# Kernel optimization log

Measured on AMD Instinct MI355X. Metric: run time of the kernel, lower is better.

## Reference

```python
import jax, jax.numpy as jnp
import numpy as np

N_NODES = 100000
N_EDGES = 1600000
FEATURE = 128
HIDDEN = 128
CLASSES = 64


def _sage_conv(x, src, dst, W_l, b_l, W_r, num_nodes):
    # mean aggregation of source-node features at destination nodes
    msgs = x[src]                                            # [E, F]
    agg = jax.ops.segment_sum(msgs, dst, num_segments=num_nodes)   # [N, F]
    cnt = jax.ops.segment_sum(jnp.ones((src.shape[0],), x.dtype), dst,
                              num_segments=num_nodes)        # [N]
    mean = agg / jnp.maximum(cnt, 1.0)[:, None]              # zero for isolated nodes
    return mean @ W_l.T + b_l + x @ W_r.T


def setup_inputs() -> dict:
    key = jax.random.key(0)
    ks = jax.random.split(key, 8)
    x = jax.random.normal(ks[0], (N_NODES, FEATURE), dtype=jnp.float32)
    edge_index = jax.random.randint(ks[1], (2, N_EDGES), 0, N_NODES, dtype=jnp.int64)
    s1 = 1.0 / np.sqrt(FEATURE)
    s2 = 1.0 / np.sqrt(HIDDEN)
    W1l = jax.random.uniform(ks[2], (HIDDEN, FEATURE), jnp.float32, -s1, s1)
    b1l = jnp.zeros((HIDDEN,), jnp.float32)
    W1r = jax.random.uniform(ks[3], (HIDDEN, FEATURE), jnp.float32, -s1, s1)
    W2l = jax.random.uniform(ks[4], (CLASSES, HIDDEN), jnp.float32, -s2, s2)
    b2l = jnp.zeros((CLASSES,), jnp.float32)
    W2r = jax.random.uniform(ks[5], (CLASSES, HIDDEN), jnp.float32, -s2, s2)
    return {"x": x, "edge_index": edge_index,
            "W1l": W1l, "b1l": b1l, "W1r": W1r,
            "W2l": W2l, "b2l": b2l, "W2r": W2r}


def reference(x, edge_index, W1l, b1l, W1r, W2l, b2l, W2r):
    src, dst = edge_index[0], edge_index[1]
    h = _sage_conv(x, src, dst, W1l, b1l, W1r, N_NODES)
    h = jax.nn.relu(h)
    # F.dropout(training=False) is identity in eval mode
    out = _sage_conv(h, src, dst, W2l, b2l, W2r, N_NODES)
    return jax.nn.log_softmax(out, axis=1)
```

## Files before the change

### kernel.cpp

```cpp
#include <hip/hip_runtime.h>

#define NF 128
#define NC 64
#define NBA 640
#define NBKT 196
#define CAP 10240
#define CAPE 12288

typedef short short8 __attribute__((ext_vector_type(8)));
typedef unsigned short ushort;
typedef float f32x4 __attribute__((ext_vector_type(4)));
typedef float f32x2 __attribute__((ext_vector_type(2)));
typedef unsigned int uint;
typedef unsigned char uchar;

__device__ __forceinline__ ushort f2b(float x) {
  unsigned u = __builtin_bit_cast(unsigned, x);
  u += 0x7fffu + ((u >> 16) & 1u);
  return (ushort)(u >> 16);
}

__global__ __launch_bounds__(256) void prep_kernel(
    const float* __restrict__ x, ushort* __restrict__ xb,
    uchar* __restrict__ x8, int n4, int nb_cast,
    const float* __restrict__ W1l, const float* __restrict__ W1r,
    ushort* __restrict__ Wp1,
    const float* __restrict__ W2l, const float* __restrict__ W2r,
    ushort* __restrict__ Wp2l, ushort* __restrict__ Wp2r,
    const int* __restrict__ src, const int* __restrict__ dst,
    int* __restrict__ gcnt, uint* __restrict__ tmp, int nE, int epb) {
  __shared__ int lh[NBKT];
  __shared__ int base[NBKT];
  int b = blockIdx.x;
  if (b < nb_cast) {
    int i = b * 256 + threadIdx.x;
    if (i >= n4) return;
    float4 v = ((const float4*)x)[i];
    ushort4 o;
    o.x = f2b(v.x); o.y = f2b(v.y); o.z = f2b(v.z); o.w = f2b(v.w);
    ((ushort4*)xb)[i] = o;
    int u = __builtin_amdgcn_cvt_pk_fp8_f32(v.x, v.y, 0, false);
    u = __builtin_amdgcn_cvt_pk_fp8_f32(v.z, v.w, u, true);
    ((uint*)x8)[i] = (uint)u;
  } else if (b < nb_cast + 128) {
    int tid = (b - nb_cast) * 256 + threadIdx.x;
    int j = tid & 7;
    int lane = (tid >> 3) & 63;
    int tile = tid >> 9;
    int nt = tile & 7, kt = tile >> 3;
    int k = kt * 32 + ((lane >> 4) << 3) + j;
    int n = nt * 16 + (lane & 15);
    float v = (k < 128) ? W1l[n * 128 + k] : W1r[n * 128 + (k - 128)];
    Wp1[tid] = f2b(v);
  } else if (b < nb_cast + 192) {
    int tid0 = (b - nb_cast - 128) * 256 + threadIdx.x;
    int which = tid0 >> 13;
    int tid = tid0 & 8191;
    int j = tid & 7;
    int lane = (tid >> 3) & 63;
    int tile = tid >> 9;
    int nt = tile & 3, kt = tile >> 2;
    int k = kt * 32 + ((lane >> 4) << 3) + j;
    int n = nt * 16 + (lane & 15);
    const float* W = which ? W2r : W2l;
    ushort* Wp = which ? Wp2r : Wp2l;
    Wp[tid] = f2b(W[n * 128 + k]);
  } else {
    int blk = b - nb_cast - 192;
    const int t = threadIdx.x;
    for (int i = t; i < NBKT; i += 256) lh[i] = 0;
    __syncthreads();
    int s0 = blk * epb, s1 = min(nE, s0 + epb);
    for (int e = s0 + t; e < s1; e += 256) atomicAdd(&lh[dst[e] >> 9], 1);
    __syncthreads();
    for (int i = t; i < NBKT; i += 256) {
      int c = lh[i];
      base[i] = c ? atomicAdd(&gcnt[i], c) : 0;
      lh[i] = 0;
    }
    __syncthreads();
    for (int e = s0 + t; e < s1; e += 256) {
      int d = dst[e];
      int s = src[e];
      int bb = d >> 9;
      int r = atomicAdd(&lh[bb], 1);
      tmp[(size_t)bb * CAP + base[bb] + r] = ((uint)(d & 511) << 17) | (uint)s;
    }
  }
}

__global__ __launch_bounds__(256) void bsortB2_kernel(
    const uint* __restrict__ tmp, const int* __restrict__ gcnt,
    int* __restrict__ esrc, int* __restrict__ deg, int* __restrict__ off,
    int nN) {
  const int bkt = blockIdx.x;
  const int t = threadIdx.x;
  __shared__ int lh[512];
  __shared__ int cur[512];
  __shared__ int wsum[4];
  const int cnt = gcnt[bkt];
  const uint* tp = tmp + (size_t)bkt * CAP;
  const int ebase = bkt * CAPE;
  lh[t] = 0;
  lh[t + 256] = 0;
  __syncthreads();
  for (int i = t; i < cnt; i += 256) atomicAdd(&lh[tp[i] >> 17], 1);
  __syncthreads();
  int v0 = lh[2 * t], v1 = lh[2 * t + 1];
  int p0 = (v0 + 3) & ~3, p1 = (v1 + 3) & ~3;
  int ts = p0 + p1;
  int lane = t & 63, wid = t >> 6;
  int x = ts;
#pragma unroll
  for (int d = 1; d < 64; d <<= 1) {
    int y = __shfl_up(x, d);
    if (lane >= d) x += y;
  }
  if (lane == 63) wsum[wid] = x;
  __syncthreads();
  int wb = 0;
  for (int w = 0; w < wid; ++w) wb += wsum[w];
  int ex = wb + x - ts;
  cur[2 * t] = ex;
  cur[2 * t + 1] = ex + p0;
  int n0 = (bkt << 9) + 2 * t, n1 = n0 + 1;
  if (n0 < nN) { off[n0] = ebase + ex;      deg[n0] = v0; }
  if (n1 < nN) { off[n1] = ebase + ex + p0; deg[n1] = v1; }
  __syncthreads();
  for (int i = t; i < cnt; i += 256) {
    uint e = tp[i];
    int r = atomicAdd(&cur[e >> 17], 1);
    esrc[ebase + r] = (int)(e & 0x1FFFFu);
  }
}

__global__ __launch_bounds__(256) void gather1_kernel(
    const uchar* __restrict__ x8, const int* __restrict__ esrc,
    const int* __restrict__ off, const int* __restrict__ deg,
    ushort* __restrict__ aggm, int nN) {
  const int w = (blockIdx.x * blockDim.x + threadIdx.x) >> 4;
  const int l = threadIdx.x & 15;
  if (w >= nN) return;
  const int o = off[w];
  const int d = deg[w];
  const uint2* __restrict__ xp = (const uint2*)x8;
  f32x2 a0 = {}, a1 = {}, a2 = {}, a3 = {};
  int i = 0;
  for (; i + 8 <= d; i += 8) {
    int4 e0 = *(const int4*)(esrc + o + i);
    int4 e1 = *(const int4*)(esrc + o + i + 4);
    uint2 v0 = xp[(size_t)e0.x * 16 + l];
    uint2 v1 = xp[(size_t)e0.y * 16 + l];
    uint2 v2 = xp[(size_t)e0.z * 16 + l];
    uint2 v3 = xp[(size_t)e0.w * 16 + l];
    uint2 v4 = xp[(size_t)e1.x * 16 + l];
    uint2 v5 = xp[(size_t)e1.y * 16 + l];
    uint2 v6 = xp[(size_t)e1.z * 16 + l];
    uint2 v7 = xp[(size_t)e1.w * 16 + l];
    a0 += ((__builtin_amdgcn_cvt_pk_f32_fp8(v0.x, false) +
            __builtin_amdgcn_cvt_pk_f32_fp8(v1.x, false)) +
           (__builtin_amdgcn_cvt_pk_f32_fp8(v2.x, false) +
            __builtin_amdgcn_cvt_pk_f32_fp8(v3.x, false))) +
          ((__builtin_amdgcn_cvt_pk_f32_fp8(v4.x, false) +
            __builtin_amdgcn_cvt_pk_f32_fp8(v5.x, false)) +
           (__builtin_amdgcn_cvt_pk_f32_fp8(v6.x, false) +
            __builtin_amdgcn_cvt_pk_f32_fp8(v7.x, false)));
    a1 += ((__builtin_amdgcn_cvt_pk_f32_fp8(v0.x, true) +
            __builtin_amdgcn_cvt_pk_f32_fp8(v1.x, true)) +
           (__builtin_amdgcn_cvt_pk_f32_fp8(v2.x, true) +
            __builtin_amdgcn_cvt_pk_f32_fp8(v3.x, true))) +
          ((__builtin_amdgcn_cvt_pk_f32_fp8(v4.x, true) +
            __builtin_amdgcn_cvt_pk_f32_fp8(v5.x, true)) +
           (__builtin_amdgcn_cvt_pk_f32_fp8(v6.x, true) +
            __builtin_amdgcn_cvt_pk_f32_fp8(v7.x, true)));
    a2 += ((__builtin_amdgcn_cvt_pk_f32_fp8(v0.y, false) +
            __builtin_amdgcn_cvt_pk_f32_fp8(v1.y, false)) +
           (__builtin_amdgcn_cvt_pk_f32_fp8(v2.y, false) +
            __builtin_amdgcn_cvt_pk_f32_fp8(v3.y, false))) +
          ((__builtin_amdgcn_cvt_pk_f32_fp8(v4.y, false) +
            __builtin_amdgcn_cvt_pk_f32_fp8(v5.y, false)) +
           (__builtin_amdgcn_cvt_pk_f32_fp8(v6.y, false) +
            __builtin_amdgcn_cvt_pk_f32_fp8(v7.y, false)));
    a3 += ((__builtin_amdgcn_cvt_pk_f32_fp8(v0.y, true) +
            __builtin_amdgcn_cvt_pk_f32_fp8(v1.y, true)) +
           (__builtin_amdgcn_cvt_pk_f32_fp8(v2.y, true) +
            __builtin_amdgcn_cvt_pk_f32_fp8(v3.y, true))) +
          ((__builtin_amdgcn_cvt_pk_f32_fp8(v4.y, true) +
            __builtin_amdgcn_cvt_pk_f32_fp8(v5.y, true)) +
           (__builtin_amdgcn_cvt_pk_f32_fp8(v6.y, true) +
            __builtin_amdgcn_cvt_pk_f32_fp8(v7.y, true)));
  }
  for (; i + 4 <= d; i += 4) {
    int4 e0 = *(const int4*)(esrc + o + i);
    uint2 v0 = xp[(size_t)e0.x * 16 + l];
    uint2 v1 = xp[(size_t)e0.y * 16 + l];
    uint2 v2 = xp[(size_t)e0.z * 16 + l];
    uint2 v3 = xp[(size_t)e0.w * 16 + l];
    a0 += (__builtin_amdgcn_cvt_pk_f32_fp8(v0.x, false) +
           __builtin_amdgcn_cvt_pk_f32_fp8(v1.x, false)) +
          (__builtin_amdgcn_cvt_pk_f32_fp8(v2.x, false) +
           __builtin_amdgcn_cvt_pk_f32_fp8(v3.x, false));
    a1 += (__builtin_amdgcn_cvt_pk_f32_fp8(v0.x, true) +
           __builtin_amdgcn_cvt_pk_f32_fp8(v1.x, true)) +
          (__builtin_amdgcn_cvt_pk_f32_fp8(v2.x, true) +
           __builtin_amdgcn_cvt_pk_f32_fp8(v3.x, true));
    a2 += (__builtin_amdgcn_cvt_pk_f32_fp8(v0.y, false) +
           __builtin_amdgcn_cvt_pk_f32_fp8(v1.y, false)) +
          (__builtin_amdgcn_cvt_pk_f32_fp8(v2.y, false) +
           __builtin_amdgcn_cvt_pk_f32_fp8(v3.y, false));
    a3 += (__builtin_amdgcn_cvt_pk_f32_fp8(v0.y, true) +
           __builtin_amdgcn_cvt_pk_f32_fp8(v1.y, true)) +
          (__builtin_amdgcn_cvt_pk_f32_fp8(v2.y, true) +
           __builtin_amdgcn_cvt_pk_f32_fp8(v3.y, true));
  }
  for (; i < d; ++i) {
    int s = esrc[o + i];
    uint2 v = xp[(size_t)s * 16 + l];
    a0 += __builtin_amdgcn_cvt_pk_f32_fp8(v.x, false);
    a1 += __builtin_amdgcn_cvt_pk_f32_fp8(v.x, true);
    a2 += __builtin_amdgcn_cvt_pk_f32_fp8(v.y, false);
    a3 += __builtin_amdgcn_cvt_pk_f32_fp8(v.y, true);
  }
  float inv = 1.0f / fmaxf((float)d, 1.0f);
  uint4 ov;
  ov.x = (uint)f2b(a0.x * inv) | ((uint)f2b(a0.y * inv) << 16);
  ov.y = (uint)f2b(a1.x * inv) | ((uint)f2b(a1.y * inv) << 16);
  ov.z = (uint)f2b(a2.x * inv) | ((uint)f2b(a2.y * inv) << 16);
  ov.w = (uint)f2b(a3.x * inv) | ((uint)f2b(a3.y * inv) << 16);
  ((uint4*)(aggm + (size_t)w * NF))[l] = ov;
}

__global__ __launch_bounds__(256) void gather2_kernel(
    const uchar* __restrict__ z8, const int* __restrict__ esrc,
    const int* __restrict__ off, const int* __restrict__ deg,
    float* __restrict__ aggz, int nN) {
  const int w = (blockIdx.x * blockDim.x + threadIdx.x) >> 3;
  const int l = threadIdx.x & 7;
  if (w >= nN) return;
  const int o = off[w];
  const int d = deg[w];
  const uint2* __restrict__ zp = (const uint2*)z8;
  f32x2 a0 = {}, a1 = {}, a2 = {}, a3 = {};
  int i = 0;
  for (; i + 8 <= d; i += 8) {
    int4 e0 = *(const int4*)(esrc + o + i);
    int4 e1 = *(const int4*)(esrc + o + i + 4);
    uint2 v0 = zp[(size_t)e0.x * 8 + l];
    uint2 v1 = zp[(size_t)e0.y * 8 + l];
    uint2 v2 = zp[(size_t)e0.z * 8 + l];
    uint2 v3 = zp[(size_t)e0.w * 8 + l];
    uint2 v4 = zp[(size_t)e1.x * 8 + l];
    uint2 v5 = zp[(size_t)e1.y * 8 + l];
    uint2 v6 = zp[(size_t)e1.z * 8 + l];
    uint2 v7 = zp[(size_t)e1.w * 8 + l];
    a0 += ((__builtin_amdgcn_cvt_pk_f32_fp8(v0.x, false) +
            __builtin_amdgcn_cvt_pk_f32_fp8(v1.x, false)) +
           (__builtin_amdgcn_cvt_pk_f32_fp8(v2.x, false) +
            __builtin_amdgcn_cvt_pk_f32_fp8(v3.x, false))) +
          ((__builtin_amdgcn_cvt_pk_f32_fp8(v4.x, false) +
            __builtin_amdgcn_cvt_pk_f32_fp8(v5.x, false)) +
           (__builtin_amdgcn_cvt_pk_f32_fp8(v6.x, false) +
            __builtin_amdgcn_cvt_pk_f32_fp8(v7.x, false)));
    a1 += ((__builtin_amdgcn_cvt_pk_f32_fp8(v0.x, true) +
            __builtin_amdgcn_cvt_pk_f32_fp8(v1.x, true)) +
           (__builtin_amdgcn_cvt_pk_f32_fp8(v2.x, true) +
            __builtin_amdgcn_cvt_pk_f32_fp8(v3.x, true))) +
          ((__builtin_amdgcn_cvt_pk_f32_fp8(v4.x, true) +
            __builtin_amdgcn_cvt_pk_f32_fp8(v5.x, true)) +
           (__builtin_amdgcn_cvt_pk_f32_fp8(v6.x, true) +
            __builtin_amdgcn_cvt_pk_f32_fp8(v7.x, true)));
    a2 += ((__builtin_amdgcn_cvt_pk_f32_fp8(v0.y, false) +
            __builtin_amdgcn_cvt_pk_f32_fp8(v1.y, false)) +
           (__builtin_amdgcn_cvt_pk_f32_fp8(v2.y, false) +
            __builtin_amdgcn_cvt_pk_f32_fp8(v3.y, false))) +
          ((__builtin_amdgcn_cvt_pk_f32_fp8(v4.y, false) +
            __builtin_amdgcn_cvt_pk_f32_fp8(v5.y, false)) +
           (__builtin_amdgcn_cvt_pk_f32_fp8(v6.y, false) +
            __builtin_amdgcn_cvt_pk_f32_fp8(v7.y, false)));
    a3 += ((__builtin_amdgcn_cvt_pk_f32_fp8(v0.y, true) +
            __builtin_amdgcn_cvt_pk_f32_fp8(v1.y, true)) +
           (__builtin_amdgcn_cvt_pk_f32_fp8(v2.y, true) +
            __builtin_amdgcn_cvt_pk_f32_fp8(v3.y, true))) +
          ((__builtin_amdgcn_cvt_pk_f32_fp8(v4.y, true) +
            __builtin_amdgcn_cvt_pk_f32_fp8(v5.y, true)) +
           (__builtin_amdgcn_cvt_pk_f32_fp8(v6.y, true) +
            __builtin_amdgcn_cvt_pk_f32_fp8(v7.y, true)));
  }
  for (; i + 4 <= d; i += 4) {
    int4 e0 = *(const int4*)(esrc + o + i);
    uint2 v0 = zp[(size_t)e0.x * 8 + l];
    uint2 v1 = zp[(size_t)e0.y * 8 + l];
    uint2 v2 = zp[(size_t)e0.z * 8 + l];
    uint2 v3 = zp[(size_t)e0.w * 8 + l];
    a0 += (__builtin_amdgcn_cvt_pk_f32_fp8(v0.x, false) +
           __builtin_amdgcn_cvt_pk_f32_fp8(v1.x, false)) +
          (__builtin_amdgcn_cvt_pk_f32_fp8(v2.x, false) +
           __builtin_amdgcn_cvt_pk_f32_fp8(v3.x, false));
    a1 += (__builtin_amdgcn_cvt_pk_f32_fp8(v0.x, true) +
           __builtin_amdgcn_cvt_pk_f32_fp8(v1.x, true)) +
          (__builtin_amdgcn_cvt_pk_f32_fp8(v2.x, true) +
           __builtin_amdgcn_cvt_pk_f32_fp8(v3.x, true));
    a2 += (__builtin_amdgcn_cvt_pk_f32_fp8(v0.y, false) +
           __builtin_amdgcn_cvt_pk_f32_fp8(v1.y, false)) +
          (__builtin_amdgcn_cvt_pk_f32_fp8(v2.y, false) +
           __builtin_amdgcn_cvt_pk_f32_fp8(v3.y, false));
    a3 += (__builtin_amdgcn_cvt_pk_f32_fp8(v0.y, true) +
           __builtin_amdgcn_cvt_pk_f32_fp8(v1.y, true)) +
          (__builtin_amdgcn_cvt_pk_f32_fp8(v2.y, true) +
           __builtin_amdgcn_cvt_pk_f32_fp8(v3.y, true));
  }
  for (; i < d; ++i) {
    int s = esrc[o + i];
    uint2 v = zp[(size_t)s * 8 + l];
    a0 += __builtin_amdgcn_cvt_pk_f32_fp8(v.x, false);
    a1 += __builtin_amdgcn_cvt_pk_f32_fp8(v.x, true);
    a2 += __builtin_amdgcn_cvt_pk_f32_fp8(v.y, false);
    a3 += __builtin_amdgcn_cvt_pk_f32_fp8(v.y, true);
  }
  float inv = 1.0f / fmaxf((float)d, 1.0f);
  ((float4*)(aggz + (size_t)w * NC))[2 * l] =
      make_float4(a0.x * inv, a0.y * inv, a1.x * inv, a1.y * inv);
  ((float4*)(aggz + (size_t)w * NC))[2 * l + 1] =
      make_float4(a2.x * inv, a2.y * inv, a3.x * inv, a3.y * inv);
}

__global__ __launch_bounds__(256) void layer12_mfma(
    const ushort* __restrict__ xb, const ushort* __restrict__ aggb,
    const ushort* __restrict__ Wp1, const float* __restrict__ b1,
    const ushort* __restrict__ Wp2l,
    ushort* __restrict__ hb, uchar* __restrict__ z8, int nN) {
  const int t = threadIdx.x;
  const int wv = t >> 6;
  const int lane = t & 63;
  const int base = blockIdx.x * 64;
  __shared__ ushort As[64][264];
  for (int i = t; i < 64 * 32; i += 256) {
    int r = i >> 5, cq = i & 31;
    int node = base + r;
    short8 v = {};
    if (node < nN) {
      const ushort* sp = (cq < 16) ? (aggb + (size_t)node * NF + cq * 8)
                                   : (xb + (size_t)node * NF + (cq - 16) * 8);
      v = *(const short8*)sp;
    }
    *(short8*)&As[r][cq * 8] = v;
  }
  __syncthreads();

  f32x4 acc[8] = {};
  const int arow = wv * 16 + (lane & 15);
  const int kq = (lane >> 4) * 8;
#pragma unroll
  for (int kt = 0; kt < 8; ++kt) {
    short8 af = *(const short8*)&As[arow][kt * 32 + kq];
#pragma unroll
    for (int nt = 0; nt < 8; ++nt) {
      short8 bf = *(const short8*)(Wp1 + ((size_t)(kt * 8 + nt) * 64 + lane) * 8);
      acc[nt] = __builtin_amdgcn_mfma_f32_16x16x32_bf16(af, bf, acc[nt], 0, 0, 0);
    }
  }
  const int quad = lane >> 4;
  const int cl = lane & 15;
#pragma unroll
  for (int nt = 0; nt < 8; ++nt) {
    float bj = b1[nt * 16 + cl];
#pragma unroll
    for (int r = 0; r < 4; ++r) {
      int node = base + wv * 16 + quad * 4 + r;
      ushort hv = f2b(fmaxf(acc[nt][r] + bj, 0.0f));
      As[wv * 16 + quad * 4 + r][nt * 16 + cl] = hv;
      if (node < nN) hb[(size_t)node * NF + nt * 16 + cl] = hv;
    }
  }

  f32x4 acc2[4] = {};
#pragma unroll
  for (int kt = 0; kt < 4; ++kt) {
    short8 af = *(const short8*)&As[arow][kt * 32 + kq];
#pragma unroll
    for (int nt = 0; nt < 4; ++nt) {
      short8 bf = *(const short8*)(Wp2l + ((size_t)(kt * 4 + nt) * 64 + lane) * 8);
      acc2[nt] = __builtin_amdgcn_mfma_f32_16x16x32_bf16(af, bf, acc2[nt], 0, 0, 0);
    }
  }
#pragma unroll
  for (int r = 0; r < 4; ++r) {
    int node = base + wv * 16 + quad * 4 + r;
    if (node < nN) {
      int u = __builtin_amdgcn_cvt_pk_fp8_f32(acc2[0][r], acc2[1][r], 0, false);
      u = __builtin_amdgcn_cvt_pk_fp8_f32(acc2[2][r], acc2[3][r], u, true);
      ((uint*)(z8 + (size_t)node * NC))[cl] = (uint)u;
    }
  }
}

__global__ __launch_bounds__(256) void layer2b_mfma(
    const ushort* __restrict__ hb, const float* __restrict__ aggz,
    const ushort* __restrict__ Wp, const float* __restrict__ b2,
    float* __restrict__ out, int nN) {
  const int t = threadIdx.x;
  const int wv = t >> 6;
  const int lane = t & 63;
  const int base = blockIdx.x * 64;
  __shared__ ushort As[64][136];
  for (int i = t; i < 64 * 16; i += 256) {
    int r = i >> 4, cq = i & 15;
    int node = base + r;
    short8 v = {};
    if (node < nN) v = *(const short8*)(hb + (size_t)node * NF + cq * 8);
    *(short8*)&As[r][cq * 8] = v;
  }
  __syncthreads();

  f32x4 acc[4] = {};
  const int arow = wv * 16 + (lane & 15);
  const int kq = (lane >> 4) * 8;
#pragma unroll
  for (int kt = 0; kt < 4; ++kt) {
    short8 af = *(const short8*)&As[arow][kt * 32 + kq];
#pragma unroll
    for (int nt = 0; nt < 4; ++nt) {
      short8 bf = *(const short8*)(Wp + ((size_t)(kt * 4 + nt) * 64 + lane) * 8);
      acc[nt] = __builtin_amdgcn_mfma_f32_16x16x32_bf16(af, bf, acc[nt], 0, 0, 0);
    }
  }
  const int quad = lane >> 4;
  const int cl = lane & 15;
  float bj[4];
#pragma unroll
  for (int nt = 0; nt < 4; ++nt) bj[nt] = b2[nt * 16 + cl];

#pragma unroll
  for (int r = 0; r < 4; ++r) {
    int node = base + wv * 16 + quad * 4 + r;
    int nvalid = (node < nN);
    float a0 = 0.f, a1 = 0.f, a2 = 0.f, a3 = 0.f;
    if (nvalid) {
      float4 av = ((const float4*)(aggz + (size_t)node * NC))[cl];
      a0 = av.x; a1 = av.y; a2 = av.z; a3 = av.w;
    }
    float v0 = acc[0][r] + bj[0] + a0;
    float v1 = acc[1][r] + bj[1] + a1;
    float v2 = acc[2][r] + bj[2] + a2;
    float v3 = acc[3][r] + bj[3] + a3;
    float mx = fmaxf(fmaxf(v0, v1), fmaxf(v2, v3));
#pragma unroll
    for (int s = 1; s < 16; s <<= 1) mx = fmaxf(mx, __shfl_xor(mx, s));
    float sm = expf(v0 - mx) + expf(v1 - mx) + expf(v2 - mx) + expf(v3 - mx);
#pragma unroll
    for (int s = 1; s < 16; s <<= 1) sm += __shfl_xor(sm, s);
    float ls = mx + logf(sm);
    if (nvalid) {
      float* op = out + (size_t)node * NC;
      op[0 * 16 + cl] = v0 - ls;
      op[1 * 16 + cl] = v1 - ls;
      op[2 * 16 + cl] = v2 - ls;
      op[3 * 16 + cl] = v3 - ls;
    }
  }
}

extern "C" void kernel_launch(void* const* d_in, const int* in_sizes, int n_in,
                              void* d_out, int out_size, void* d_ws, size_t ws_size,
                              hipStream_t stream) {
  const float* x   = (const float*)d_in[0];
  const int*   ei  = (const int*)d_in[1];
  const float* W1l = (const float*)d_in[2];
  const float* b1l = (const float*)d_in[3];
  const float* W1r = (const float*)d_in[4];
  const float* W2l = (const float*)d_in[5];
  const float* b2l = (const float*)d_in[6];
  const float* W2r = (const float*)d_in[7];
  float* out = (float*)d_out;

  const int nN = in_sizes[0] / NF;
  const int nE = in_sizes[1] / 2;
  const int* src = ei;
  const int* dst = ei + nE;

  char* p = (char*)d_ws;
  ushort* xb   = (ushort*)p; p += (size_t)nN * NF * 2;
  ushort* hb   = (ushort*)p; p += (size_t)nN * NF * 2;
  ushort* aggb = (ushort*)p; p += (size_t)nN * NF * 2;
  ushort* Wp1  = (ushort*)p; p += 256 * 128 * 2;
  ushort* Wp2l = (ushort*)p; p += 128 * 64 * 2;
  ushort* Wp2r = (ushort*)p; p += 128 * 64 * 2;
  int* gcnt    = (int*)p;    p += 1024;
  int* deg     = (int*)p;    p += (size_t)nN * 4;
  int* off     = (int*)p;    p += (size_t)nN * 4;
  uint* tmp    = (uint*)p;   p += (size_t)NBKT * CAP * 4;
  int* esrc    = (int*)p;    p += (size_t)NBKT * CAPE * 4;
  uchar* z8buf = (uchar*)p;  p += (size_t)nN * NC;

  uchar* x8   = (uchar*)hb;
  uchar* z8   = z8buf;
  float* aggz = (float*)aggb;

  const int n4 = nN * NF / 4;
  const int nb_cast = (n4 + 255) / 256;
  const int epb = (nE + NBA - 1) / NBA;

  hipMemsetAsync(gcnt, 0, NBKT * sizeof(int), stream);

  prep_kernel<<<nb_cast + 192 + NBA, 256, 0, stream>>>(
      x, xb, x8, n4, nb_cast, W1l, W1r, Wp1, W2l, W2r, Wp2l, Wp2r,
      src, dst, gcnt, tmp, nE, epb);

  bsortB2_kernel<<<NBKT, 256, 0, stream>>>(tmp, gcnt, esrc, deg, off, nN);

  gather1_kernel<<<(nN * 16 + 255) / 256, 256, 0, stream>>>(x8, esrc, off, deg, aggb, nN);
  layer12_mfma<<<(nN + 63) / 64, 256, 0, stream>>>(xb, aggb, Wp1, b1l, Wp2l, hb, z8, nN);

  gather2_kernel<<<(nN * 8 + 255) / 256, 256, 0, stream>>>(z8, esrc, off, deg, aggz, nN);
  layer2b_mfma<<<(nN + 63) / 64, 256, 0, stream>>>(hb, aggz, Wp2r, b2l, out, nN);
}
```

Baseline: 275.8 us.

## Fuse neighbor gathers into the MFMA layer kernels via shared memory

Removes the two standalone gather kernels and performs each mean aggregation inside the matching MFMA layer kernel. Each block writes its 64 rows of aggregated features straight into LDS instead of through a global intermediate buffer. This drops two launches and the global write/read round-trip of the aggregates. It also moves the edge-bucketing blocks to the front of prep_kernel so they get scheduled first. The cost is that each block now mixes latency-bound gathers with MFMA work, with fewer threads per node and more LDS use (an extra float tile in layer 2), which may lower occupancy.

```diff
diff --git a/kernel.cpp b/kernel.cpp
--- a/kernel.cpp
+++ b/kernel.cpp
@@ -32,8 +32,29 @@
   __shared__ int lh[NBKT];
   __shared__ int base[NBKT];
   int b = blockIdx.x;
-  if (b < nb_cast) {
-    int i = b * 256 + threadIdx.x;
+  if (b < NBA) {
+    int blk = b;
+    const int t = threadIdx.x;
+    for (int i = t; i < NBKT; i += 256) lh[i] = 0;
+    __syncthreads();
+    int s0 = blk * epb, s1 = min(nE, s0 + epb);
+    for (int e = s0 + t; e < s1; e += 256) atomicAdd(&lh[dst[e] >> 9], 1);
+    __syncthreads();
+    for (int i = t; i < NBKT; i += 256) {
+      int c = lh[i];
+      base[i] = c ? atomicAdd(&gcnt[i], c) : 0;
+      lh[i] = 0;
+    }
+    __syncthreads();
+    for (int e = s0 + t; e < s1; e += 256) {
+      int d = dst[e];
+      int s = src[e];
+      int bb = d >> 9;
+      int r = atomicAdd(&lh[bb], 1);
+      tmp[(size_t)bb * CAP + base[bb] + r] = ((uint)(d & 511) << 17) | (uint)s;
+    }
+  } else if (b < NBA + nb_cast) {
+    int i = (b - NBA) * 256 + threadIdx.x;
     if (i >= n4) return;
     float4 v = ((const float4*)x)[i];
     ushort4 o;
@@ -42,8 +63,8 @@
     int u = __builtin_amdgcn_cvt_pk_fp8_f32(v.x, v.y, 0, false);
     u = __builtin_amdgcn_cvt_pk_fp8_f32(v.z, v.w, u, true);
     ((uint*)x8)[i] = (uint)u;
-  } else if (b < nb_cast + 128) {
-    int tid = (b - nb_cast) * 256 + threadIdx.x;
+  } else if (b < NBA + nb_cast + 128) {
+    int tid = (b - NBA - nb_cast) * 256 + threadIdx.x;
     int j = tid & 7;
     int lane = (tid >> 3) & 63;
     int tile = tid >> 9;
@@ -52,8 +73,8 @@
     int n = nt * 16 + (lane & 15);
     float v = (k < 128) ? W1l[n * 128 + k] : W1r[n * 128 + (k - 128)];
     Wp1[tid] = f2b(v);
-  } else if (b < nb_cast + 192) {
-    int tid0 = (b - nb_cast - 128) * 256 + threadIdx.x;
+  } else {
+    int tid0 = (b - NBA - nb_cast - 128) * 256 + threadIdx.x;
     int which = tid0 >> 13;
     int tid = tid0 & 8191;
     int j = tid & 7;
@@ -65,27 +86,6 @@
     const float* W = which ? W2r : W2l;
     ushort* Wp = which ? Wp2r : Wp2l;
     Wp[tid] = f2b(W[n * 128 + k]);
-  } else {
-    int blk = b - nb_cast - 192;
-    const int t = threadIdx.x;
-    for (int i = t; i < NBKT; i += 256) lh[i] = 0;
-    __syncthreads();
-    int s0 = blk * epb, s1 = min(nE, s0 + epb);
-    for (int e = s0 + t; e < s1; e += 256) atomicAdd(&lh[dst[e] >> 9], 1);
-    __syncthreads();
-    for (int i = t; i < NBKT; i += 256) {
-      int c = lh[i];
-      base[i] = c ? atomicAdd(&gcnt[i], c) : 0;
-      lh[i] = 0;
-    }
-    __syncthreads();
-    for (int e = s0 + t; e < s1; e += 256) {
-      int d = dst[e];
-      int s = src[e];
-      int bb = d >> 9;
-      int r = atomicAdd(&lh[bb], 1);
-      tmp[(size_t)bb * CAP + base[bb] + r] = ((uint)(d & 511) << 17) | (uint)s;
-    }
   }
 }
 
@@ -134,198 +134,10 @@
   }
 }
 
-__global__ __launch_bounds__(256) void gather1_kernel(
-    const uchar* __restrict__ x8, const int* __restrict__ esrc,
-    const int* __restrict__ off, const int* __restrict__ deg,
-    ushort* __restrict__ aggm, int nN) {
-  const int w = (blockIdx.x * blockDim.x + threadIdx.x) >> 4;
-  const int l = threadIdx.x & 15;
-  if (w >= nN) return;
-  const int o = off[w];
-  const int d = deg[w];
-  const uint2* __restrict__ xp = (const uint2*)x8;
-  f32x2 a0 = {}, a1 = {}, a2 = {}, a3 = {};
-  int i = 0;
-  for (; i + 8 <= d; i += 8) {
-    int4 e0 = *(const int4*)(esrc + o + i);
-    int4 e1 = *(const int4*)(esrc + o + i + 4);
-    uint2 v0 = xp[(size_t)e0.x * 16 + l];
-    uint2 v1 = xp[(size_t)e0.y * 16 + l];
-    uint2 v2 = xp[(size_t)e0.z * 16 + l];
-    uint2 v3 = xp[(size_t)e0.w * 16 + l];
-    uint2 v4 = xp[(size_t)e1.x * 16 + l];
-    uint2 v5 = xp[(size_t)e1.y * 16 + l];
-    uint2 v6 = xp[(size_t)e1.z * 16 + l];
-    uint2 v7 = xp[(size_t)e1.w * 16 + l];
-    a0 += ((__builtin_amdgcn_cvt_pk_f32_fp8(v0.x, false) +
-            __builtin_amdgcn_cvt_pk_f32_fp8(v1.x, false)) +
-           (__builtin_amdgcn_cvt_pk_f32_fp8(v2.x, false) +
-            __builtin_amdgcn_cvt_pk_f32_fp8(v3.x, false))) +
-          ((__builtin_amdgcn_cvt_pk_f32_fp8(v4.x, false) +
-            __builtin_amdgcn_cvt_pk_f32_fp8(v5.x, false)) +
-           (__builtin_amdgcn_cvt_pk_f32_fp8(v6.x, false) +
-            __builtin_amdgcn_cvt_pk_f32_fp8(v7.x, false)));
-    a1 += ((__builtin_amdgcn_cvt_pk_f32_fp8(v0.x, true) +
-            __builtin_amdgcn_cvt_pk_f32_fp8(v1.x, true)) +
-           (__builtin_amdgcn_cvt_pk_f32_fp8(v2.x, true) +
-            __builtin_amdgcn_cvt_pk_f32_fp8(v3.x, true))) +
-          ((__builtin_amdgcn_cvt_pk_f32_fp8(v4.x, true) +
-            __builtin_amdgcn_cvt_pk_f32_fp8(v5.x, true)) +
-           (__builtin_amdgcn_cvt_pk_f32_fp8(v6.x, true) +
-            __builtin_amdgcn_cvt_pk_f32_fp8(v7.x, true)));
-    a2 += ((__builtin_amdgcn_cvt_pk_f32_fp8(v0.y, false) +
-            __builtin_amdgcn_cvt_pk_f32_fp8(v1.y, false)) +
-           (__builtin_amdgcn_cvt_pk_f32_fp8(v2.y, false) +
-            __builtin_amdgcn_cvt_pk_f32_fp8(v3.y, false))) +
-          ((__builtin_amdgcn_cvt_pk_f32_fp8(v4.y, false) +
-            __builtin_amdgcn_cvt_pk_f32_fp8(v5.y, false)) +
-           (__builtin_amdgcn_cvt_pk_f32_fp8(v6.y, false) +
-            __builtin_amdgcn_cvt_pk_f32_fp8(v7.y, false)));
-    a3 += ((__builtin_amdgcn_cvt_pk_f32_fp8(v0.y, true) +
-            __builtin_amdgcn_cvt_pk_f32_fp8(v1.y, true)) +
-           (__builtin_amdgcn_cvt_pk_f32_fp8(v2.y, true) +
-            __builtin_amdgcn_cvt_pk_f32_fp8(v3.y, true))) +
-          ((__builtin_amdgcn_cvt_pk_f32_fp8(v4.y, true) +
-            __builtin_amdgcn_cvt_pk_f32_fp8(v5.y, true)) +
-           (__builtin_amdgcn_cvt_pk_f32_fp8(v6.y, true) +
-            __builtin_amdgcn_cvt_pk_f32_fp8(v7.y, true)));
-  }
-  for (; i + 4 <= d; i += 4) {
-    int4 e0 = *(const int4*)(esrc + o + i);
-    uint2 v0 = xp[(size_t)e0.x * 16 + l];
-    uint2 v1 = xp[(size_t)e0.y * 16 + l];
-    uint2 v2 = xp[(size_t)e0.z * 16 + l];
-    uint2 v3 = xp[(size_t)e0.w * 16 + l];
-    a0 += (__builtin_amdgcn_cvt_pk_f32_fp8(v0.x, false) +
-           __builtin_amdgcn_cvt_pk_f32_fp8(v1.x, false)) +
-          (__builtin_amdgcn_cvt_pk_f32_fp8(v2.x, false) +
-           __builtin_amdgcn_cvt_pk_f32_fp8(v3.x, false));
-    a1 += (__builtin_amdgcn_cvt_pk_f32_fp8(v0.x, true) +
-           __builtin_amdgcn_cvt_pk_f32_fp8(v1.x, true)) +
-          (__builtin_amdgcn_cvt_pk_f32_fp8(v2.x, true) +
-           __builtin_amdgcn_cvt_pk_f32_fp8(v3.x, true));
-    a2 += (__builtin_amdgcn_cvt_pk_f32_fp8(v0.y, false) +
-           __builtin_amdgcn_cvt_pk_f32_fp8(v1.y, false)) +
-          (__builtin_amdgcn_cvt_pk_f32_fp8(v2.y, false) +
-           __builtin_amdgcn_cvt_pk_f32_fp8(v3.y, false));
-    a3 += (__builtin_amdgcn_cvt_pk_f32_fp8(v0.y, true) +
-           __builtin_amdgcn_cvt_pk_f32_fp8(v1.y, true)) +
-          (__builtin_amdgcn_cvt_pk_f32_fp8(v2.y, true) +
-           __builtin_amdgcn_cvt_pk_f32_fp8(v3.y, true));
-  }
-  for (; i < d; ++i) {
-    int s = esrc[o + i];
-    uint2 v = xp[(size_t)s * 16 + l];
-    a0 += __builtin_amdgcn_cvt_pk_f32_fp8(v.x, false);
-    a1 += __builtin_amdgcn_cvt_pk_f32_fp8(v.x, true);
-    a2 += __builtin_amdgcn_cvt_pk_f32_fp8(v.y, false);
-    a3 += __builtin_amdgcn_cvt_pk_f32_fp8(v.y, true);
-  }
-  float inv = 1.0f / fmaxf((float)d, 1.0f);
-  uint4 ov;
-  ov.x = (uint)f2b(a0.x * inv) | ((uint)f2b(a0.y * inv) << 16);
-  ov.y = (uint)f2b(a1.x * inv) | ((uint)f2b(a1.y * inv) << 16);
-  ov.z = (uint)f2b(a2.x * inv) | ((uint)f2b(a2.y * inv) << 16);
-  ov.w = (uint)f2b(a3.x * inv) | ((uint)f2b(a3.y * inv) << 16);
-  ((uint4*)(aggm + (size_t)w * NF))[l] = ov;
-}
-
-__global__ __launch_bounds__(256) void gather2_kernel(
-    const uchar* __restrict__ z8, const int* __restrict__ esrc,
-    const int* __restrict__ off, const int* __restrict__ deg,
-    float* __restrict__ aggz, int nN) {
-  const int w = (blockIdx.x * blockDim.x + threadIdx.x) >> 3;
-  const int l = threadIdx.x & 7;
-  if (w >= nN) return;
-  const int o = off[w];
-  const int d = deg[w];
-  const uint2* __restrict__ zp = (const uint2*)z8;
-  f32x2 a0 = {}, a1 = {}, a2 = {}, a3 = {};
-  int i = 0;
-  for (; i + 8 <= d; i += 8) {
-    int4 e0 = *(const int4*)(esrc + o + i);
-    int4 e1 = *(const int4*)(esrc + o + i + 4);
-    uint2 v0 = zp[(size_t)e0.x * 8 + l];
-    uint2 v1 = zp[(size_t)e0.y * 8 + l];
-    uint2 v2 = zp[(size_t)e0.z * 8 + l];
-    uint2 v3 = zp[(size_t)e0.w * 8 + l];
-    uint2 v4 = zp[(size_t)e1.x * 8 + l];
-    uint2 v5 = zp[(size_t)e1.y * 8 + l];
-    uint2 v6 = zp[(size_t)e1.z * 8 + l];
-    uint2 v7 = zp[(size_t)e1.w * 8 + l];
-    a0 += ((__builtin_amdgcn_cvt_pk_f32_fp8(v0.x, false) +
-            __builtin_amdgcn_cvt_pk_f32_fp8(v1.x, false)) +
-           (__builtin_amdgcn_cvt_pk_f32_fp8(v2.x, false) +
-            __builtin_amdgcn_cvt_pk_f32_fp8(v3.x, false))) +
-          ((__builtin_amdgcn_cvt_pk_f32_fp8(v4.x, false) +
-            __builtin_amdgcn_cvt_pk_f32_fp8(v5.x, false)) +
-           (__builtin_amdgcn_cvt_pk_f32_fp8(v6.x, false) +
-            __builtin_amdgcn_cvt_pk_f32_fp8(v7.x, false)));
-    a1 += ((__builtin_amdgcn_cvt_pk_f32_fp8(v0.x, true) +
-            __builtin_amdgcn_cvt_pk_f32_fp8(v1.x, true)) +
-           (__builtin_amdgcn_cvt_pk_f32_fp8(v2.x, true) +
-            __builtin_amdgcn_cvt_pk_f32_fp8(v3.x, true))) +
-          ((__builtin_amdgcn_cvt_pk_f32_fp8(v4.x, true) +
-            __builtin_amdgcn_cvt_pk_f32_fp8(v5.x, true)) +
-           (__builtin_amdgcn_cvt_pk_f32_fp8(v6.x, true) +
-            __builtin_amdgcn_cvt_pk_f32_fp8(v7.x, true)));
-    a2 += ((__builtin_amdgcn_cvt_pk_f32_fp8(v0.y, false) +
-            __builtin_amdgcn_cvt_pk_f32_fp8(v1.y, false)) +
-           (__builtin_amdgcn_cvt_pk_f32_fp8(v2.y, false) +
-            __builtin_amdgcn_cvt_pk_f32_fp8(v3.y, false))) +
-          ((__builtin_amdgcn_cvt_pk_f32_fp8(v4.y, false) +
-            __builtin_amdgcn_cvt_pk_f32_fp8(v5.y, false)) +
-           (__builtin_amdgcn_cvt_pk_f32_fp8(v6.y, false) +
-            __builtin_amdgcn_cvt_pk_f32_fp8(v7.y, false)));
-    a3 += ((__builtin_amdgcn_cvt_pk_f32_fp8(v0.y, true) +
-            __builtin_amdgcn_cvt_pk_f32_fp8(v1.y, true)) +
-           (__builtin_amdgcn_cvt_pk_f32_fp8(v2.y, true) +
-            __builtin_amdgcn_cvt_pk_f32_fp8(v3.y, true))) +
-          ((__builtin_amdgcn_cvt_pk_f32_fp8(v4.y, true) +
-            __builtin_amdgcn_cvt_pk_f32_fp8(v5.y, true)) +
-           (__builtin_amdgcn_cvt_pk_f32_fp8(v6.y, true) +
-            __builtin_amdgcn_cvt_pk_f32_fp8(v7.y, true)));
-  }
-  for (; i + 4 <= d; i += 4) {
-    int4 e0 = *(const int4*)(esrc + o + i);
-    uint2 v0 = zp[(size_t)e0.x * 8 + l];
-    uint2 v1 = zp[(size_t)e0.y * 8 + l];
-    uint2 v2 = zp[(size_t)e0.z * 8 + l];
-    uint2 v3 = zp[(size_t)e0.w * 8 + l];
-    a0 += (__builtin_amdgcn_cvt_pk_f32_fp8(v0.x, false) +
-           __builtin_amdgcn_cvt_pk_f32_fp8(v1.x, false)) +
-          (__builtin_amdgcn_cvt_pk_f32_fp8(v2.x, false) +
-           __builtin_amdgcn_cvt_pk_f32_fp8(v3.x, false));
-    a1 += (__builtin_amdgcn_cvt_pk_f32_fp8(v0.x, true) +
-           __builtin_amdgcn_cvt_pk_f32_fp8(v1.x, true)) +
-          (__builtin_amdgcn_cvt_pk_f32_fp8(v2.x, true) +
-           __builtin_amdgcn_cvt_pk_f32_fp8(v3.x, true));
-    a2 += (__builtin_amdgcn_cvt_pk_f32_fp8(v0.y, false) +
-           __builtin_amdgcn_cvt_pk_f32_fp8(v1.y, false)) +
-          (__builtin_amdgcn_cvt_pk_f32_fp8(v2.y, false) +
-           __builtin_amdgcn_cvt_pk_f32_fp8(v3.y, false));
-    a3 += (__builtin_amdgcn_cvt_pk_f32_fp8(v0.y, true) +
-           __builtin_amdgcn_cvt_pk_f32_fp8(v1.y, true)) +
-          (__builtin_amdgcn_cvt_pk_f32_fp8(v2.y, true) +
-           __builtin_amdgcn_cvt_pk_f32_fp8(v3.y, true));
-  }
-  for (; i < d; ++i) {
-    int s = esrc[o + i];
-    uint2 v = zp[(size_t)s * 8 + l];
-    a0 += __builtin_amdgcn_cvt_pk_f32_fp8(v.x, false);
-    a1 += __builtin_amdgcn_cvt_pk_f32_fp8(v.x, true);
-    a2 += __builtin_amdgcn_cvt_pk_f32_fp8(v.y, false);
-    a3 += __builtin_amdgcn_cvt_pk_f32_fp8(v.y, true);
-  }
-  float inv = 1.0f / fmaxf((float)d, 1.0f);
-  ((float4*)(aggz + (size_t)w * NC))[2 * l] =
-      make_float4(a0.x * inv, a0.y * inv, a1.x * inv, a1.y * inv);
-  ((float4*)(aggz + (size_t)w * NC))[2 * l + 1] =
-      make_float4(a2.x * inv, a2.y * inv, a3.x * inv, a3.y * inv);
-}
-
 __global__ __launch_bounds__(256) void layer12_mfma(
-    const ushort* __restrict__ xb, const ushort* __restrict__ aggb,
+    const uchar* __restrict__ x8, const ushort* __restrict__ xb,
+    const int* __restrict__ esrc, const int* __restrict__ off,
+    const int* __restrict__ deg,
     const ushort* __restrict__ Wp1, const float* __restrict__ b1,
     const ushort* __restrict__ Wp2l,
     ushort* __restrict__ hb, uchar* __restrict__ z8, int nN) {
@@ -334,16 +146,109 @@
   const int lane = t & 63;
   const int base = blockIdx.x * 64;
   __shared__ ushort As[64][264];
-  for (int i = t; i < 64 * 32; i += 256) {
-    int r = i >> 5, cq = i & 31;
+
+  for (int i = t; i < 64 * 16; i += 256) {
+    int r = i >> 4, cq = i & 15;
     int node = base + r;
     short8 v = {};
-    if (node < nN) {
-      const ushort* sp = (cq < 16) ? (aggb + (size_t)node * NF + cq * 8)
-                                   : (xb + (size_t)node * NF + (cq - 16) * 8);
-      v = *(const short8*)sp;
-    }
-    *(short8*)&As[r][cq * 8] = v;
+    if (node < nN) v = *(const short8*)(xb + (size_t)node * NF + cq * 8);
+    *(short8*)&As[r][128 + cq * 8] = v;
+  }
+
+  {
+    const int g = t >> 4;
+    const int l = t & 15;
+    const uint2* __restrict__ xp = (const uint2*)x8;
+    for (int k = 0; k < 4; ++k) {
+      int r = g * 4 + k;
+      int node = base + r;
+      int o = 0, d = 0;
+      if (node < nN) { o = off[node]; d = deg[node]; }
+      f32x2 a0 = {}, a1 = {}, a2 = {}, a3 = {};
+      int i = 0;
+      for (; i + 8 <= d; i += 8) {
+        int4 e0 = *(const int4*)(esrc + o + i);
+        int4 e1 = *(const int4*)(esrc + o + i + 4);
+        uint2 v0 = xp[(size_t)e0.x * 16 + l];
+        uint2 v1 = xp[(size_t)e0.y * 16 + l];
+        uint2 v2 = xp[(size_t)e0.z * 16 + l];
+        uint2 v3 = xp[(size_t)e0.w * 16 + l];
+        uint2 v4 = xp[(size_t)e1.x * 16 + l];
+        uint2 v5 = xp[(size_t)e1.y * 16 + l];
+        uint2 v6 = xp[(size_t)e1.z * 16 + l];
+        uint2 v7 = xp[(size_t)e1.w * 16 + l];
+        a0 += ((__builtin_amdgcn_cvt_pk_f32_fp8(v0.x, false) +
+                __builtin_amdgcn_cvt_pk_f32_fp8(v1.x, false)) +
+               (__builtin_amdgcn_cvt_pk_f32_fp8(v2.x, false) +
+                __builtin_amdgcn_cvt_pk_f32_fp8(v3.x, false))) +
+              ((__builtin_amdgcn_cvt_pk_f32_fp8(v4.x, false) +
+                __builtin_amdgcn_cvt_pk_f32_fp8(v5.x, false)) +
+               (__builtin_amdgcn_cvt_pk_f32_fp8(v6.x, false) +
+                __builtin_amdgcn_cvt_pk_f32_fp8(v7.x, false)));
+        a1 += ((__builtin_amdgcn_cvt_pk_f32_fp8(v0.x, true) +
+                __builtin_amdgcn_cvt_pk_f32_fp8(v1.x, true)) +
+               (__builtin_amdgcn_cvt_pk_f32_fp8(v2.x, true) +
+                __builtin_amdgcn_cvt_pk_f32_fp8(v3.x, true))) +
+              ((__builtin_amdgcn_cvt_pk_f32_fp8(v4.x, true) +
+                __builtin_amdgcn_cvt_pk_f32_fp8(v5.x, true)) +
+               (__builtin_amdgcn_cvt_pk_f32_fp8(v6.x, true) +
+                __builtin_amdgcn_cvt_pk_f32_fp8(v7.x, true)));
+        a2 += ((__builtin_amdgcn_cvt_pk_f32_fp8(v0.y, false) +
+                __builtin_amdgcn_cvt_pk_f32_fp8(v1.y, false)) +
+               (__builtin_amdgcn_cvt_pk_f32_fp8(v2.y, false) +
+                __builtin_amdgcn_cvt_pk_f32_fp8(v3.y, false))) +
+              ((__builtin_amdgcn_cvt_pk_f32_fp8(v4.y, false) +
+                __builtin_amdgcn_cvt_pk_f32_fp8(v5.y, false)) +
+               (__builtin_amdgcn_cvt_pk_f32_fp8(v6.y, false) +
+                __builtin_amdgcn_cvt_pk_f32_fp8(v7.y, false)));
+        a3 += ((__builtin_amdgcn_cvt_pk_f32_fp8(v0.y, true) +
+                __builtin_amdgcn_cvt_pk_f32_fp8(v1.y, true)) +
+               (__builtin_amdgcn_cvt_pk_f32_fp8(v2.y, true) +
+                __builtin_amdgcn_cvt_pk_f32_fp8(v3.y, true))) +
+              ((__builtin_amdgcn_cvt_pk_f32_fp8(v4.y, true) +
+                __builtin_amdgcn_cvt_pk_f32_fp8(v5.y, true)) +
+               (__builtin_amdgcn_cvt_pk_f32_fp8(v6.y, true) +
+                __builtin_amdgcn_cvt_pk_f32_fp8(v7.y, true)));
+      }
+      for (; i + 4 <= d; i += 4) {
+        int4 e0 = *(const int4*)(esrc + o + i);
+        uint2 v0 = xp[(size_t)e0.x * 16 + l];
+        uint2 v1 = xp[(size_t)e0.y * 16 + l];
+        uint2 v2 = xp[(size_t)e0.z * 16 + l];
+        uint2 v3 = xp[(size_t)e0.w * 16 + l];
+        a0 += (__builtin_amdgcn_cvt_pk_f32_fp8(v0.x, false) +
+               __builtin_amdgcn_cvt_pk_f32_fp8(v1.x, false)) +
+              (__builtin_amdgcn_cvt_pk_f32_fp8(v2.x, false) +
+               __builtin_amdgcn_cvt_pk_f32_fp8(v3.x, false));
+        a1 += (__builtin_amdgcn_cvt_pk_f32_fp8(v0.x, true) +
+               __builtin_amdgcn_cvt_pk_f32_fp8(v1.x, true)) +
+              (__builtin_amdgcn_cvt_pk_f32_fp8(v2.x, true) +
+               __builtin_amdgcn_cvt_pk_f32_fp8(v3.x, true));
+        a2 += (__builtin_amdgcn_cvt_pk_f32_fp8(v0.y, false) +
+               __builtin_amdgcn_cvt_pk_f32_fp8(v1.y, false)) +
+              (__builtin_amdgcn_cvt_pk_f32_fp8(v2.y, false) +
+               __builtin_amdgcn_cvt_pk_f32_fp8(v3.y, false));
+        a3 += (__builtin_amdgcn_cvt_pk_f32_fp8(v0.y, true) +
+               __builtin_amdgcn_cvt_pk_f32_fp8(v1.y, true)) +
+              (__builtin_amdgcn_cvt_pk_f32_fp8(v2.y, true) +
+               __builtin_amdgcn_cvt_pk_f32_fp8(v3.y, true));
+      }
+      for (; i < d; ++i) {
+        int s = esrc[o + i];
+        uint2 v = xp[(size_t)s * 16 + l];
+        a0 += __builtin_amdgcn_cvt_pk_f32_fp8(v.x, false);
+        a1 += __builtin_amdgcn_cvt_pk_f32_fp8(v.x, true);
+        a2 += __builtin_amdgcn_cvt_pk_f32_fp8(v.y, false);
+        a3 += __builtin_amdgcn_cvt_pk_f32_fp8(v.y, true);
+      }
+      float inv = 1.0f / fmaxf((float)d, 1.0f);
+      uint4 ov;
+      ov.x = (uint)f2b(a0.x * inv) | ((uint)f2b(a0.y * inv) << 16);
+      ov.y = (uint)f2b(a1.x * inv) | ((uint)f2b(a1.y * inv) << 16);
+      ov.z = (uint)f2b(a2.x * inv) | ((uint)f2b(a2.y * inv) << 16);
+      ov.w = (uint)f2b(a3.x * inv) | ((uint)f2b(a3.y * inv) << 16);
+      *(uint4*)&As[r][l * 8] = ov;
+    }
   }
   __syncthreads();
 
@@ -395,7 +300,9 @@
 }
 
 __global__ __launch_bounds__(256) void layer2b_mfma(
-    const ushort* __restrict__ hb, const float* __restrict__ aggz,
+    const ushort* __restrict__ hb, const uchar* __restrict__ z8,
+    const int* __restrict__ esrc, const int* __restrict__ off,
+    const int* __restrict__ deg,
     const ushort* __restrict__ Wp, const float* __restrict__ b2,
     float* __restrict__ out, int nN) {
   const int t = threadIdx.x;
@@ -403,6 +310,8 @@
   const int lane = t & 63;
   const int base = blockIdx.x * 64;
   __shared__ ushort As[64][136];
+  __shared__ float Az[64][68];
+
   for (int i = t; i < 64 * 16; i += 256) {
     int r = i >> 4, cq = i & 15;
     int node = base + r;
@@ -410,6 +319,100 @@
     if (node < nN) v = *(const short8*)(hb + (size_t)node * NF + cq * 8);
     *(short8*)&As[r][cq * 8] = v;
   }
+
+  {
+    const int g8 = t >> 3;
+    const int l = t & 7;
+    const uint2* __restrict__ zp = (const uint2*)z8;
+    for (int k = 0; k < 2; ++k) {
+      int r = g8 * 2 + k;
+      int node = base + r;
+      int o = 0, d = 0;
+      if (node < nN) { o = off[node]; d = deg[node]; }
+      f32x2 a0 = {}, a1 = {}, a2 = {}, a3 = {};
+      int i = 0;
+      for (; i + 8 <= d; i += 8) {
+        int4 e0 = *(const int4*)(esrc + o + i);
+        int4 e1 = *(const int4*)(esrc + o + i + 4);
+        uint2 v0 = zp[(size_t)e0.x * 8 + l];
+        uint2 v1 = zp[(size_t)e0.y * 8 + l];
+        uint2 v2 = zp[(size_t)e0.z * 8 + l];
+        uint2 v3 = zp[(size_t)e0.w * 8 + l];
+        uint2 v4 = zp[(size_t)e1.x * 8 + l];
+        uint2 v5 = zp[(size_t)e1.y * 8 + l];
+        uint2 v6 = zp[(size_t)e1.z * 8 + l];
+        uint2 v7 = zp[(size_t)e1.w * 8 + l];
+        a0 += ((__builtin_amdgcn_cvt_pk_f32_fp8(v0.x, false) +
+                __builtin_amdgcn_cvt_pk_f32_fp8(v1.x, false)) +
+               (__builtin_amdgcn_cvt_pk_f32_fp8(v2.x, false) +
+                __builtin_amdgcn_cvt_pk_f32_fp8(v3.x, false))) +
+              ((__builtin_amdgcn_cvt_pk_f32_fp8(v4.x, false) +
+                __builtin_amdgcn_cvt_pk_f32_fp8(v5.x, false)) +
+               (__builtin_amdgcn_cvt_pk_f32_fp8(v6.x, false) +
+                __builtin_amdgcn_cvt_pk_f32_fp8(v7.x, false)));
+        a1 += ((__builtin_amdgcn_cvt_pk_f32_fp8(v0.x, true) +
+                __builtin_amdgcn_cvt_pk_f32_fp8(v1.x, true)) +
+               (__builtin_amdgcn_cvt_pk_f32_fp8(v2.x, true) +
+                __builtin_amdgcn_cvt_pk_f32_fp8(v3.x, true))) +
+              ((__builtin_amdgcn_cvt_pk_f32_fp8(v4.x, true) +
+                __builtin_amdgcn_cvt_pk_f32_fp8(v5.x, true)) +
+               (__builtin_amdgcn_cvt_pk_f32_fp8(v6.x, true) +
+                __builtin_amdgcn_cvt_pk_f32_fp8(v7.x, true)));
+        a2 += ((__builtin_amdgcn_cvt_pk_f32_fp8(v0.y, false) +
+                __builtin_amdgcn_cvt_pk_f32_fp8(v1.y, false)) +
+               (__builtin_amdgcn_cvt_pk_f32_fp8(v2.y, false) +
+                __builtin_amdgcn_cvt_pk_f32_fp8(v3.y, false))) +
+              ((__builtin_amdgcn_cvt_pk_f32_fp8(v4.y, false) +
+                __builtin_amdgcn_cvt_pk_f32_fp8(v5.y, false)) +
+               (__builtin_amdgcn_cvt_pk_f32_fp8(v6.y, false) +
+                __builtin_amdgcn_cvt_pk_f32_fp8(v7.y, false)));
+        a3 += ((__builtin_amdgcn_cvt_pk_f32_fp8(v0.y, true) +
+                __builtin_amdgcn_cvt_pk_f32_fp8(v1.y, true)) +
+               (__builtin_amdgcn_cvt_pk_f32_fp8(v2.y, true) +
+                __builtin_amdgcn_cvt_pk_f32_fp8(v3.y, true))) +
+              ((__builtin_amdgcn_cvt_pk_f32_fp8(v4.y, true) +
+                __builtin_amdgcn_cvt_pk_f32_fp8(v5.y, true)) +
+               (__builtin_amdgcn_cvt_pk_f32_fp8(v6.y, true) +
+                __builtin_amdgcn_cvt_pk_f32_fp8(v7.y, true)));
+      }
+      for (; i + 4 <= d; i += 4) {
+        int4 e0 = *(const int4*)(esrc + o + i);
+        uint2 v0 = zp[(size_t)e0.x * 8 + l];
+        uint2 v1 = zp[(size_t)e0.y * 8 + l];
+        uint2 v2 = zp[(size_t)e0.z * 8 + l];
+        uint2 v3 = zp[(size_t)e0.w * 8 + l];
+        a0 += (__builtin_amdgcn_cvt_pk_f32_fp8(v0.x, false) +
+               __builtin_amdgcn_cvt_pk_f32_fp8(v1.x, false)) +
+              (__builtin_amdgcn_cvt_pk_f32_fp8(v2.x, false) +
+               __builtin_amdgcn_cvt_pk_f32_fp8(v3.x, false));
+        a1 += (__builtin_amdgcn_cvt_pk_f32_fp8(v0.x, true) +
+               __builtin_amdgcn_cvt_pk_f32_fp8(v1.x, true)) +
+              (__builtin_amdgcn_cvt_pk_f32_fp8(v2.x, true) +
+               __builtin_amdgcn_cvt_pk_f32_fp8(v3.x, true));
+        a2 += (__builtin_amdgcn_cvt_pk_f32_fp8(v0.y, false) +
+               __builtin_amdgcn_cvt_pk_f32_fp8(v1.y, false)) +
+              (__builtin_amdgcn_cvt_pk_f32_fp8(v2.y, false) +
+               __builtin_amdgcn_cvt_pk_f32_fp8(v3.y, false));
+        a3 += (__builtin_amdgcn_cvt_pk_f32_fp8(v0.y, true) +
+               __builtin_amdgcn_cvt_pk_f32_fp8(v1.y, true)) +
+              (__builtin_amdgcn_cvt_pk_f32_fp8(v2.y, true) +
+               __builtin_amdgcn_cvt_pk_f32_fp8(v3.y, true));
+      }
+      for (; i < d; ++i) {
+        int s = esrc[o + i];
+        uint2 v = zp[(size_t)s * 8 + l];
+        a0 += __builtin_amdgcn_cvt_pk_f32_fp8(v.x, false);
+        a1 += __builtin_amdgcn_cvt_pk_f32_fp8(v.x, true);
+        a2 += __builtin_amdgcn_cvt_pk_f32_fp8(v.y, false);
+        a3 += __builtin_amdgcn_cvt_pk_f32_fp8(v.y, true);
+      }
+      float inv = 1.0f / fmaxf((float)d, 1.0f);
+      *(float4*)&Az[r][8 * l] =
+          make_float4(a0.x * inv, a0.y * inv, a1.x * inv, a1.y * inv);
+      *(float4*)&Az[r][8 * l + 4] =
+          make_float4(a2.x * inv, a2.y * inv, a3.x * inv, a3.y * inv);
+    }
+  }
   __syncthreads();
 
   f32x4 acc[4] = {};
@@ -432,17 +435,14 @@
 
 #pragma unroll
   for (int r = 0; r < 4; ++r) {
-    int node = base + wv * 16 + quad * 4 + r;
+    int rr = wv * 16 + quad * 4 + r;
+    int node = base + rr;
     int nvalid = (node < nN);
-    float a0 = 0.f, a1 = 0.f, a2 = 0.f, a3 = 0.f;
-    if (nvalid) {
-      float4 av = ((const float4*)(aggz + (size_t)node * NC))[cl];
-      a0 = av.x; a1 = av.y; a2 = av.z; a3 = av.w;
-    }
-    float v0 = acc[0][r] + bj[0] + a0;
-    float v1 = acc[1][r] + bj[1] + a1;
-    float v2 = acc[2][r] + bj[2] + a2;
-    float v3 = acc[3][r] + bj[3] + a3;
+    float4 av = *(const float4*)&Az[rr][4 * cl];
+    float v0 = acc[0][r] + bj[0] + av.x;
+    float v1 = acc[1][r] + bj[1] + av.y;
+    float v2 = acc[2][r] + bj[2] + av.z;
+    float v3 = acc[3][r] + bj[3] + av.w;
     float mx = fmaxf(fmaxf(v0, v1), fmaxf(v2, v3));
 #pragma unroll
     for (int s = 1; s < 16; s <<= 1) mx = fmaxf(mx, __shfl_xor(mx, s));
@@ -480,8 +480,8 @@
 
   char* p = (char*)d_ws;
   ushort* xb   = (ushort*)p; p += (size_t)nN * NF * 2;
+  uchar*  x8   = (uchar*)p;  p += (size_t)nN * NF;
   ushort* hb   = (ushort*)p; p += (size_t)nN * NF * 2;
-  ushort* aggb = (ushort*)p; p += (size_t)nN * NF * 2;
   ushort* Wp1  = (ushort*)p; p += 256 * 128 * 2;
   ushort* Wp2l = (ushort*)p; p += 128 * 64 * 2;
   ushort* Wp2r = (ushort*)p; p += 128 * 64 * 2;
@@ -490,11 +490,7 @@
   int* off     = (int*)p;    p += (size_t)nN * 4;
   uint* tmp    = (uint*)p;   p += (size_t)NBKT * CAP * 4;
   int* esrc    = (int*)p;    p += (size_t)NBKT * CAPE * 4;
-  uchar* z8buf = (uchar*)p;  p += (size_t)nN * NC;
-
-  uchar* x8   = (uchar*)hb;
-  uchar* z8   = z8buf;
-  float* aggz = (float*)aggb;
+  uchar* z8    = (uchar*)p;  p += (size_t)nN * NC;
 
   const int n4 = nN * NF / 4;
   const int nb_cast = (n4 + 255) / 256;
@@ -502,15 +498,15 @@
 
   hipMemsetAsync(gcnt, 0, NBKT * sizeof(int), stream);
 
-  prep_kernel<<<nb_cast + 192 + NBA, 256, 0, stream>>>(
+  prep_kernel<<<NBA + nb_cast + 192, 256, 0, stream>>>(
       x, xb, x8, n4, nb_cast, W1l, W1r, Wp1, W2l, W2r, Wp2l, Wp2r,
       src, dst, gcnt, tmp, nE, epb);
 
   bsortB2_kernel<<<NBKT, 256, 0, stream>>>(tmp, gcnt, esrc, deg, off, nN);
 
-  gather1_kernel<<<(nN * 16 + 255) / 256, 256, 0, stream>>>(x8, esrc, off, deg, aggb, nN);
-  layer12_mfma<<<(nN + 63) / 64, 256, 0, stream>>>(xb, aggb, Wp1, b1l, Wp2l, hb, z8, nN);
-
-  gather2_kernel<<<(nN * 8 + 255) / 256, 256, 0, stream>>>(z8, esrc, off, deg, aggz, nN);
-  layer2b_mfma<<<(nN + 63) / 64, 256, 0, stream>>>(hb, aggz, Wp2r, b2l, out, nN);
+  layer12_mfma<<<(nN + 63) / 64, 256, 0, stream>>>(
+      x8, xb, esrc, off, deg, Wp1, b1l, Wp2l, hb, z8, nN);
+
+  layer2b_mfma<<<(nN + 63) / 64, 256, 0, stream>>>(
+      hb, z8, esrc, off, deg, Wp2r, b2l, out, nN);
 }
```

After: 294.6 us. 6.8% more time.
